# Optimization experiments

Measured on AMD Instinct MI355X. Metric: run time of the kernel, lower is better.

## Reference

```python
import jax, jax.numpy as jnp
import numpy as np

N = 50000      # atoms
E = 800000     # edges (avg degree 32)
H = 64         # hidden_channels
F = 64         # num_filters
G = 50         # num_gaussians
L = 6          # num_interactions
B = 128        # graphs in batch
MAX_Z = 100
CUTOFF = 10.0


def setup_inputs() -> dict:
    key = jax.random.key(0)
    ks = jax.random.split(key, 20)
    s = 0.05  # weight scale
    return {
        "z": jax.random.randint(ks[0], (N,), 0, MAX_Z, dtype=jnp.int32),
        "pos": jax.random.uniform(ks[1], (N, 3), dtype=jnp.float32) * 5.0,
        "batch": jnp.sort(jax.random.randint(ks[2], (N,), 0, B, dtype=jnp.int32)),
        "edge_index": jax.random.randint(ks[3], (2, E), 0, N, dtype=jnp.int32),
        "embed": jax.random.normal(ks[4], (MAX_Z, H), dtype=jnp.float32) * s,
        "mlp_w1": jax.random.normal(ks[5], (L, G, F), dtype=jnp.float32) * s,
        "mlp_b1": jax.random.normal(ks[6], (L, F), dtype=jnp.float32) * s,
        "mlp_w2": jax.random.normal(ks[7], (L, F, F), dtype=jnp.float32) * s,
        "mlp_b2": jax.random.normal(ks[8], (L, F), dtype=jnp.float32) * s,
        "lin_w": jax.random.normal(ks[9], (L, H, F), dtype=jnp.float32) * s,
        "lin_out_w": jax.random.normal(ks[10], (L, F, H), dtype=jnp.float32) * s,
        "lin_out_b": jax.random.normal(ks[11], (L, H), dtype=jnp.float32) * s,
        "fc1_w": jax.random.normal(ks[12], (H, H // 2), dtype=jnp.float32) * s,
        "fc1_b": jax.random.normal(ks[13], (H // 2,), dtype=jnp.float32) * s,
        "fc2_w": jax.random.normal(ks[14], (H // 2, 1), dtype=jnp.float32) * s,
        "fc2_b": jax.random.normal(ks[15], (1,), dtype=jnp.float32) * s,
    }


def reference(z, pos, batch, edge_index, embed, mlp_w1, mlp_b1, mlp_w2, mlp_b2,
              lin_w, lin_out_w, lin_out_b, fc1_w, fc1_b, fc2_w, fc2_b):
    src, dst = edge_index[0], edge_index[1]
    # edge distances (replaces the python cdist loop; edge list is precomputed)
    d = jnp.sqrt(jnp.sum((pos[src] - pos[dst]) ** 2, axis=-1))  # [E]
    # Gaussian smearing
    offset = jnp.linspace(0.0, CUTOFF, G)
    coeff = -0.5 / (offset[1] - offset[0]) ** 2
    edge_attr = jnp.exp(coeff * (d[:, None] - offset) ** 2)  # [E, G]
    # cosine cutoff
    cut = 0.5 * (jnp.cos(d * np.pi / CUTOFF) + 1.0) * (d < CUTOFF).astype(d.dtype)  # [E]

    h = embed[z]  # [N, H]
    for l in range(L):
        # filter MLP on edge features, modulated by cutoff
        W = jnp.tanh(edge_attr @ mlp_w1[l] + mlp_b1[l]) @ mlp_w2[l] + mlp_b2[l]  # [E, F]
        W = W * cut[:, None]
        h_j = h @ lin_w[l]  # [N, F]
        messages = h_j[src] * W  # gather + modulate  [E, F]
        agg = jax.ops.segment_sum(messages, dst, num_segments=N)  # scatter-add [N, F]
        h = h + (agg @ lin_out_w[l] + lin_out_b[l])  # residual

    # global mean pool over graphs
    sums = jax.ops.segment_sum(h, batch, num_segments=B)  # [B, H]
    cnt = jax.ops.segment_sum(jnp.ones((h.shape[0],), h.dtype), batch, num_segments=B)
    pooled = sums / jnp.maximum(cnt, 1.0)[:, None]

    x = jax.nn.relu(pooled @ fc1_w + fc1_b)  # dropout = identity (eval)
    return x @ fc2_w + fc2_b  # [B, 1]
```

## Files before the change

### kernel.cpp

```cpp
#include <hip/hip_runtime.h>
#include <math.h>

#define E_EDGES 800000
#define N_ATOMS 50000
#define N_GRAPH 128
#define P_TBL   4096
#define SCAN_NB 49

static constexpr float PI_F   = 3.14159265358979323846f;
static constexpr float GSTEP  = 10.0f / 49.0f;
static constexpr float GCOEFF = -0.5f / (GSTEP * GSTEP);
static constexpr float DMAX   = 8.6603f;
static constexpr float DSCALE = (float)(P_TBL - 1) / DMAX;

__global__ void hist_kernel(const int* __restrict__ dst, int* __restrict__ cnt) {
    int e = blockIdx.x * 256 + threadIdx.x;
    if (e < E_EDGES) atomicAdd(&cnt[dst[e]], 1);
}

__global__ __launch_bounds__(1024)
void scan1_kernel(const int* __restrict__ cnt, int* __restrict__ local_ex,
                  int* __restrict__ bsum) {
    __shared__ int sh[1024];
    const int t = threadIdx.x;
    const int i = blockIdx.x * 1024 + t;
    const int v = (i < N_ATOMS) ? cnt[i] : 0;
    sh[t] = v;
    __syncthreads();
    #pragma unroll
    for (int off = 1; off < 1024; off <<= 1) {
        int u = (t >= off) ? sh[t - off] : 0;
        __syncthreads();
        sh[t] += u;
        __syncthreads();
    }
    if (i < N_ATOMS) local_ex[i] = sh[t] - v;
    if (t == 1023) bsum[blockIdx.x] = sh[t];
}

__global__ __launch_bounds__(1024)
void scan2_kernel(const int* __restrict__ local_ex, const int* __restrict__ bsum,
                  int* __restrict__ starts, int* __restrict__ cursor) {
    __shared__ int off;
    const int b = blockIdx.x;
    if (threadIdx.x < 64) {
        int v = (threadIdx.x < b) ? bsum[threadIdx.x] : 0;
        #pragma unroll
        for (int d = 32; d > 0; d >>= 1) v += __shfl_down(v, d, 64);
        if (threadIdx.x == 0) off = v;
    }
    __syncthreads();
    const int i = b * 1024 + threadIdx.x;
    if (i < N_ATOMS) {
        int v = local_ex[i] + off;
        starts[i] = v;
        cursor[i] = v;
    }
}

__global__ void scatter_kernel(const int* __restrict__ ei, const float* __restrict__ pos,
                               int* __restrict__ cursor, uint2* __restrict__ pk) {
    int e = blockIdx.x * 256 + threadIdx.x;
    if (e >= E_EDGES) return;
    int sidx = ei[e];
    int dd   = ei[E_EDGES + e];
    float dx = pos[3*sidx+0] - pos[3*dd+0];
    float dy = pos[3*sidx+1] - pos[3*dd+1];
    float dz = pos[3*sidx+2] - pos[3*dd+2];
    float dist = sqrtf(dx*dx + dy*dy + dz*dz);
    int p = atomicAdd(&cursor[dd], 1);
    pk[p] = make_uint2((unsigned)sidx, __float_as_uint(dist));
}

__global__ __launch_bounds__(256)
void table_kernel(const float* __restrict__ w1, const float* __restrict__ b1,
                  const float* __restrict__ w2, const float* __restrict__ b2,
                  float* __restrict__ tbl2) {
    __shared__ float sa[4][52];
    __shared__ float st[4][64];
    const int l  = blockIdx.x >> 10;
    const int rb = blockIdx.x & 1023;
    const int rr = threadIdx.x >> 6;
    const int f  = threadIdx.x & 63;
    const int r  = rb * 4 + rr;
    const float dp = (float)r * (DMAX / (float)(P_TBL - 1));

    if (f < 50) {
        float t = dp - (float)f * GSTEP;
        sa[rr][f] = expf(GCOEFF * t * t);
    }
    __syncthreads();

    const float* W1 = w1 + (size_t)l * 50 * 64;
    const float* W2 = w2 + (size_t)l * 64 * 64;
    float t = b1[l * 64 + f];
    #pragma unroll 5
    for (int g = 0; g < 50; ++g) t = fmaf(sa[rr][g], W1[g * 64 + f], t);
    st[rr][f] = tanhf(t);
    __syncthreads();

    float w = b2[l * 64 + f];
    #pragma unroll 8
    for (int k = 0; k < 64; ++k) w = fmaf(st[rr][k], W2[k * 64 + f], w);
    float cutv = 0.5f * (cosf(dp * (PI_F / 10.0f)) + 1.0f);
    float val = w * cutv;
    const size_t base = ((size_t)l * P_TBL + r) * 64 + f;
    tbl2[base * 2 + 0] = val;
    if (r > 0) tbl2[(base - 64) * 2 + 1] = val;
}

__global__ __launch_bounds__(256)
void embed_lin0_kernel(const int* __restrict__ z, const float* __restrict__ embed,
                       const float* __restrict__ W,
                       float* __restrict__ h, float* __restrict__ hj) {
    __shared__ float sA[64 * 65];
    __shared__ float sW[64 * 64];
    const int tid = threadIdx.x;
    const int rbase = blockIdx.x * 64;

    for (int i = tid; i < 64 * 64; i += 256) sW[i] = W[i];
    for (int i = tid; i < 64 * 64; i += 256) {
        int r = i >> 6, k = i & 63;
        int row = rbase + r;
        float v = 0.0f;
        if (row < N_ATOMS) {
            v = embed[(size_t)z[row] * 64 + k];
            h[(size_t)row * 64 + k] = v;
        }
        sA[r * 65 + k] = v;
    }
    __syncthreads();

    const int f0 = (tid & 7) * 8;
    const int r0 = (tid >> 3) * 2;
    float acc[2][8];
    #pragma unroll
    for (int i = 0; i < 2; ++i)
        #pragma unroll
        for (int j = 0; j < 8; ++j) acc[i][j] = 0.0f;

    #pragma unroll 4
    for (int k = 0; k < 64; ++k) {
        float a[2] = { sA[(r0+0)*65 + k], sA[(r0+1)*65 + k] };
        float4 wa = *(const float4*)&sW[k * 64 + f0];
        float4 wb = *(const float4*)&sW[k * 64 + f0 + 4];
        float w[8] = {wa.x, wa.y, wa.z, wa.w, wb.x, wb.y, wb.z, wb.w};
        #pragma unroll
        for (int i = 0; i < 2; ++i)
            #pragma unroll
            for (int j = 0; j < 8; ++j)
                acc[i][j] = fmaf(a[i], w[j], acc[i][j]);
    }

    #pragma unroll
    for (int i = 0; i < 2; ++i) {
        int row = rbase + r0 + i;
        if (row < N_ATOMS) {
            float* o = hj + (size_t)row * 64;
            *(float4*)&o[f0]     = make_float4(acc[i][0], acc[i][1], acc[i][2], acc[i][3]);
            *(float4*)&o[f0 + 4] = make_float4(acc[i][4], acc[i][5], acc[i][6], acc[i][7]);
        }
    }
}

__device__ __forceinline__ float edge_w2(const float2* __restrict__ tbl, float dist, int f) {
    float x = dist * DSCALE;
    int i0 = (int)x; i0 = (i0 > P_TBL - 2) ? (P_TBL - 2) : i0;
    float fr = x - (float)i0;
    float2 t = tbl[i0 * 64 + f];
    return fmaf(fr, t.y - t.x, t.x);
}

__global__ __launch_bounds__(512)
void layer_kernel(const uint2* __restrict__ pk,
                  const int* __restrict__ starts, const int* __restrict__ cnts,
                  const float* __restrict__ hj_in, const float2* __restrict__ tbl,
                  const float* __restrict__ Wout, const float* __restrict__ bout,
                  float* __restrict__ h,
                  const float* __restrict__ Wlin, float* __restrict__ hj_out,
                  int doLin) {
    __shared__ float sA[64 * 65];
    __shared__ float sW1[64 * 64];
    __shared__ float sW2[64 * 64];
    __shared__ float sb[64];
    const int tid = threadIdx.x;
    const int rbase = blockIdx.x * 64;
    const int f  = tid & 63;
    const int wv = tid >> 6;
    const int r0 = tid >> 3;
    const int f0 = (tid & 7) * 8;
    const int myrow = rbase + r0;

    float4 hA = make_float4(0.f,0.f,0.f,0.f), hB = hA;
    if (myrow < N_ATOMS) {
        const float* hr = h + (size_t)myrow * 64;
        hA = *(const float4*)&hr[f0];
        hB = *(const float4*)&hr[f0 + 4];
    }

    for (int i = tid; i < 64 * 64; i += 512) sW1[i] = Wout[i];
    if (doLin)
        for (int i = tid; i < 64 * 64; i += 512) sW2[i] = Wlin[i];
    if (tid < 64) sb[tid] = bout[tid];
    __syncthreads();

    for (int i = 0; i < 8; ++i) {
        const int r = wv * 8 + i;
        const int n = rbase + r;
        float res = 0.0f;
        if (n < N_ATOMS) {
            const int s   = starts[n];
            const int end = s + cnts[n];
            float a0 = 0.0f, a1 = 0.0f, a2 = 0.0f, a3 = 0.0f;
            float a4 = 0.0f, a5 = 0.0f, a6 = 0.0f, a7 = 0.0f;
            int e = s;
            for (; e + 8 <= end; e += 8) {
                uint2 p0 = pk[e+0], p1 = pk[e+1], p2 = pk[e+2], p3 = pk[e+3];
                uint2 p4 = pk[e+4], p5 = pk[e+5], p6 = pk[e+6], p7 = pk[e+7];
                float w0 = edge_w2(tbl, __uint_as_float(p0.y), f);
                float w1 = edge_w2(tbl, __uint_as_float(p1.y), f);
                float w2 = edge_w2(tbl, __uint_as_float(p2.y), f);
                float w3 = edge_w2(tbl, __uint_as_float(p3.y), f);
                float w4 = edge_w2(tbl, __uint_as_float(p4.y), f);
                float w5 = edge_w2(tbl, __uint_as_float(p5.y), f);
                float w6 = edge_w2(tbl, __uint_as_float(p6.y), f);
                float w7 = edge_w2(tbl, __uint_as_float(p7.y), f);
                a0 = fmaf(w0, hj_in[(size_t)p0.x * 64 + f], a0);
                a1 = fmaf(w1, hj_in[(size_t)p1.x * 64 + f], a1);
                a2 = fmaf(w2, hj_in[(size_t)p2.x * 64 + f], a2);
                a3 = fmaf(w3, hj_in[(size_t)p3.x * 64 + f], a3);
                a4 = fmaf(w4, hj_in[(size_t)p4.x * 64 + f], a4);
                a5 = fmaf(w5, hj_in[(size_t)p5.x * 64 + f], a5);
                a6 = fmaf(w6, hj_in[(size_t)p6.x * 64 + f], a6);
                a7 = fmaf(w7, hj_in[(size_t)p7.x * 64 + f], a7);
            }
            for (; e + 2 <= end; e += 2) {
                uint2 p0 = pk[e], p1 = pk[e+1];
                float w0 = edge_w2(tbl, __uint_as_float(p0.y), f);
                float w1 = edge_w2(tbl, __uint_as_float(p1.y), f);
                a0 = fmaf(w0, hj_in[(size_t)p0.x * 64 + f], a0);
                a1 = fmaf(w1, hj_in[(size_t)p1.x * 64 + f], a1);
            }
            if (e < end) {
                uint2 p0 = pk[e];
                float w0 = edge_w2(tbl, __uint_as_float(p0.y), f);
                a0 = fmaf(w0, hj_in[(size_t)p0.x * 64 + f], a0);
            }
            res = ((a0 + a1) + (a2 + a3)) + ((a4 + a5) + (a6 + a7));
        }
        sA[r * 65 + f] = res;
    }
    __builtin_amdgcn_wave_barrier();

    float acc[8];
    acc[0] = hA.x + sb[f0+0]; acc[1] = hA.y + sb[f0+1];
    acc[2] = hA.z + sb[f0+2]; acc[3] = hA.w + sb[f0+3];
    acc[4] = hB.x + sb[f0+4]; acc[5] = hB.y + sb[f0+5];
    acc[6] = hB.z + sb[f0+6]; acc[7] = hB.w + sb[f0+7];

    #pragma unroll 4
    for (int k = 0; k < 64; ++k) {
        float a = sA[r0 * 65 + k];
        float4 wa = *(const float4*)&sW1[k * 64 + f0];
        float4 wb = *(const float4*)&sW1[k * 64 + f0 + 4];
        acc[0] = fmaf(a, wa.x, acc[0]); acc[1] = fmaf(a, wa.y, acc[1]);
        acc[2] = fmaf(a, wa.z, acc[2]); acc[3] = fmaf(a, wa.w, acc[3]);
        acc[4] = fmaf(a, wb.x, acc[4]); acc[5] = fmaf(a, wb.y, acc[5]);
        acc[6] = fmaf(a, wb.z, acc[6]); acc[7] = fmaf(a, wb.w, acc[7]);
    }
    __builtin_amdgcn_wave_barrier();

    if (myrow < N_ATOMS) {
        float* o = h + (size_t)myrow * 64;
        *(float4*)&o[f0]     = make_float4(acc[0], acc[1], acc[2], acc[3]);
        *(float4*)&o[f0 + 4] = make_float4(acc[4], acc[5], acc[6], acc[7]);
    }
    #pragma unroll
    for (int j = 0; j < 8; ++j) sA[r0 * 65 + f0 + j] = acc[j];
    if (!doLin) return;
    __builtin_amdgcn_wave_barrier();

    float acc2[8];
    #pragma unroll
    for (int j = 0; j < 8; ++j) acc2[j] = 0.0f;

    #pragma unroll 4
    for (int k = 0; k < 64; ++k) {
        float a = sA[r0 * 65 + k];
        float4 wa = *(const float4*)&sW2[k * 64 + f0];
        float4 wb = *(const float4*)&sW2[k * 64 + f0 + 4];
        acc2[0] = fmaf(a, wa.x, acc2[0]); acc2[1] = fmaf(a, wa.y, acc2[1]);
        acc2[2] = fmaf(a, wa.z, acc2[2]); acc2[3] = fmaf(a, wa.w, acc2[3]);
        acc2[4] = fmaf(a, wb.x, acc2[4]); acc2[5] = fmaf(a, wb.y, acc2[5]);
        acc2[6] = fmaf(a, wb.z, acc2[6]); acc2[7] = fmaf(a, wb.w, acc2[7]);
    }

    if (myrow < N_ATOMS) {
        float* o = hj_out + (size_t)myrow * 64;
        *(float4*)&o[f0]     = make_float4(acc2[0], acc2[1], acc2[2], acc2[3]);
        *(float4*)&o[f0 + 4] = make_float4(acc2[4], acc2[5], acc2[6], acc2[7]);
    }
}

__global__ __launch_bounds__(256)
void pool_head_kernel(const float* __restrict__ h, const int* __restrict__ batch,
                      const float* __restrict__ fc1w, const float* __restrict__ fc1b,
                      const float* __restrict__ fc2w, const float* __restrict__ fc2b,
                      float* __restrict__ out) {
    __shared__ float part[4][64];
    __shared__ float sp[64];
    __shared__ float sx[32];
    __shared__ int bounds[2];
    const int g   = blockIdx.x;
    const int tid = threadIdx.x;

    if (tid < 2) {
        int target = g + tid;
        int lo = 0, hi = N_ATOMS;
        while (lo < hi) {
            int m = (lo + hi) >> 1;
            if (batch[m] < target) lo = m + 1; else hi = m;
        }
        bounds[tid] = lo;
    }
    __syncthreads();
    const int s = bounds[0], epos = bounds[1];

    const int f = tid & 63, wv = tid >> 6;
    float a = 0.0f;
    for (int r = s + wv; r < epos; r += 4) a += h[(size_t)r * 64 + f];
    part[wv][f] = a;
    __syncthreads();

    if (tid < 64) {
        float cnt = (float)(epos - s);
        sp[tid] = (part[0][tid] + part[1][tid] + part[2][tid] + part[3][tid])
                  / fmaxf(cnt, 1.0f);
    }
    __syncthreads();
    if (tid < 32) {
        float a1 = fc1b[tid];
        #pragma unroll 8
        for (int k = 0; k < 64; ++k) a1 = fmaf(sp[k], fc1w[k * 32 + tid], a1);
        sx[tid] = fmaxf(a1, 0.0f);
    }
    __syncthreads();
    if (tid == 0) {
        float a2 = fc2b[0];
        #pragma unroll 8
        for (int j = 0; j < 32; ++j) a2 = fmaf(sx[j], fc2w[j], a2);
        out[g] = a2;
    }
}

extern "C" void kernel_launch(void* const* d_in, const int* in_sizes, int n_in,
                              void* d_out, int out_size, void* d_ws, size_t ws_size,
                              hipStream_t stream) {
    const int*   z         = (const int*)  d_in[0];
    const float* pos       = (const float*)d_in[1];
    const int*   batch     = (const int*)  d_in[2];
    const int*   ei        = (const int*)  d_in[3];
    const float* embed     = (const float*)d_in[4];
    const float* mlp_w1    = (const float*)d_in[5];
    const float* mlp_b1    = (const float*)d_in[6];
    const float* mlp_w2    = (const float*)d_in[7];
    const float* mlp_b2    = (const float*)d_in[8];
    const float* lin_w     = (const float*)d_in[9];
    const float* lin_out_w = (const float*)d_in[10];
    const float* lin_out_b = (const float*)d_in[11];
    const float* fc1w      = (const float*)d_in[12];
    const float* fc1b      = (const float*)d_in[13];
    const float* fc2w      = (const float*)d_in[14];
    const float* fc2b      = (const float*)d_in[15];
    float* out = (float*)d_out;

    float*  ws    = (float*)d_ws;
    float*  h     = ws;
    float*  hj0   = h     + (size_t)N_ATOMS * 64;
    float*  hj1   = hj0   + (size_t)N_ATOMS * 64;
    float2* tbl   = (float2*)(hj1 + (size_t)N_ATOMS * 64);
    uint2*  pk    = (uint2*)(tbl + (size_t)6 * P_TBL * 64);
    int*    hist  = (int*)(pk + E_EDGES);
    int*    starts= hist  + N_ATOMS;
    int*    cursor= starts+ N_ATOMS;
    int*    lex   = cursor+ N_ATOMS;
    int*    bsum  = lex   + N_ATOMS;

    const int* dst = ei + E_EDGES;

    hipMemsetAsync(hist, 0, N_ATOMS * sizeof(int), stream);
    hist_kernel<<<E_EDGES / 256, 256, 0, stream>>>(dst, hist);
    scan1_kernel<<<SCAN_NB, 1024, 0, stream>>>(hist, lex, bsum);
    scan2_kernel<<<SCAN_NB, 1024, 0, stream>>>(lex, bsum, starts, cursor);
    scatter_kernel<<<E_EDGES / 256, 256, 0, stream>>>(ei, pos, cursor, pk);
    table_kernel<<<6 * (P_TBL / 4), 256, 0, stream>>>(mlp_w1, mlp_b1, mlp_w2, mlp_b2,
                                                      (float*)tbl);

    const int ngemm_grid = (N_ATOMS + 63) / 64;

    embed_lin0_kernel<<<ngemm_grid, 256, 0, stream>>>(z, embed, lin_w, h, hj0);

    float* hjbuf[2] = { hj0, hj1 };
    for (int l = 0; l < 6; ++l) {
        layer_kernel<<<ngemm_grid, 512, 0, stream>>>(
            pk, starts, hist, hjbuf[l & 1], tbl + (size_t)l * P_TBL * 64,
            lin_out_w + (size_t)l * 64 * 64, lin_out_b + (size_t)l * 64, h,
            (l < 5) ? (lin_w + (size_t)(l + 1) * 64 * 64) : nullptr,
            hjbuf[(l + 1) & 1], (l < 5) ? 1 : 0);
    }

    pool_head_kernel<<<N_GRAPH, 256, 0, stream>>>(h, batch, fc1w, fc1b, fc2w, fc2b, out);
}
```

Before: 729.4 us.

## Store hj features in fp16 and halve the filter lookup table

The per-atom message features hj are now written as fp16 by the embed and layer kernels and widened to fp32 inside the edge gather loop. This halves the bytes moved by the random per-edge gather, which is the dominant memory traffic. The interpolated filter table also drops from 4096 to 2048 distance points, halving table build work and its cache footprint. Both changes cost accuracy: fp16 rounding of the features and coarser linear interpolation of the filter.

```diff
diff --git a/kernel.cpp b/kernel.cpp
--- a/kernel.cpp
+++ b/kernel.cpp
@@ -1,10 +1,11 @@
 #include <hip/hip_runtime.h>
+#include <hip/hip_fp16.h>
 #include <math.h>
 
 #define E_EDGES 800000
 #define N_ATOMS 50000
 #define N_GRAPH 128
-#define P_TBL   4096
+#define P_TBL   2048
 #define SCAN_NB 49
 
 static constexpr float PI_F   = 3.14159265358979323846f;
@@ -78,8 +79,8 @@
                   float* __restrict__ tbl2) {
     __shared__ float sa[4][52];
     __shared__ float st[4][64];
-    const int l  = blockIdx.x >> 10;
-    const int rb = blockIdx.x & 1023;
+    const int l  = blockIdx.x >> 9;
+    const int rb = blockIdx.x & 511;
     const int rr = threadIdx.x >> 6;
     const int f  = threadIdx.x & 63;
     const int r  = rb * 4 + rr;
@@ -109,10 +110,17 @@
     if (r > 0) tbl2[(base - 64) * 2 + 1] = val;
 }
 
+__device__ __forceinline__ void store_half8(__half* dst, const float* v) {
+    union { ushort u[8]; uint4 q; } p;
+    #pragma unroll
+    for (int j = 0; j < 8; ++j) p.u[j] = __half_as_ushort(__float2half(v[j]));
+    *(uint4*)dst = p.q;
+}
+
 __global__ __launch_bounds__(256)
 void embed_lin0_kernel(const int* __restrict__ z, const float* __restrict__ embed,
                        const float* __restrict__ W,
-                       float* __restrict__ h, float* __restrict__ hj) {
+                       float* __restrict__ h, __half* __restrict__ hj) {
     __shared__ float sA[64 * 65];
     __shared__ float sW[64 * 64];
     const int tid = threadIdx.x;
@@ -155,11 +163,8 @@
     #pragma unroll
     for (int i = 0; i < 2; ++i) {
         int row = rbase + r0 + i;
-        if (row < N_ATOMS) {
-            float* o = hj + (size_t)row * 64;
-            *(float4*)&o[f0]     = make_float4(acc[i][0], acc[i][1], acc[i][2], acc[i][3]);
-            *(float4*)&o[f0 + 4] = make_float4(acc[i][4], acc[i][5], acc[i][6], acc[i][7]);
-        }
+        if (row < N_ATOMS)
+            store_half8(hj + (size_t)row * 64 + f0, acc[i]);
     }
 }
 
@@ -174,10 +179,10 @@
 __global__ __launch_bounds__(512)
 void layer_kernel(const uint2* __restrict__ pk,
                   const int* __restrict__ starts, const int* __restrict__ cnts,
-                  const float* __restrict__ hj_in, const float2* __restrict__ tbl,
+                  const __half* __restrict__ hj_in, const float2* __restrict__ tbl,
                   const float* __restrict__ Wout, const float* __restrict__ bout,
                   float* __restrict__ h,
-                  const float* __restrict__ Wlin, float* __restrict__ hj_out,
+                  const float* __restrict__ Wlin, __half* __restrict__ hj_out,
                   int doLin) {
     __shared__ float sA[64 * 65];
     __shared__ float sW1[64 * 64];
@@ -225,26 +230,26 @@
                 float w5 = edge_w2(tbl, __uint_as_float(p5.y), f);
                 float w6 = edge_w2(tbl, __uint_as_float(p6.y), f);
                 float w7 = edge_w2(tbl, __uint_as_float(p7.y), f);
-                a0 = fmaf(w0, hj_in[(size_t)p0.x * 64 + f], a0);
-                a1 = fmaf(w1, hj_in[(size_t)p1.x * 64 + f], a1);
-                a2 = fmaf(w2, hj_in[(size_t)p2.x * 64 + f], a2);
-                a3 = fmaf(w3, hj_in[(size_t)p3.x * 64 + f], a3);
-                a4 = fmaf(w4, hj_in[(size_t)p4.x * 64 + f], a4);
-                a5 = fmaf(w5, hj_in[(size_t)p5.x * 64 + f], a5);
-                a6 = fmaf(w6, hj_in[(size_t)p6.x * 64 + f], a6);
-                a7 = fmaf(w7, hj_in[(size_t)p7.x * 64 + f], a7);
+                a0 = fmaf(w0, __half2float(hj_in[(size_t)p0.x * 64 + f]), a0);
+                a1 = fmaf(w1, __half2float(hj_in[(size_t)p1.x * 64 + f]), a1);
+                a2 = fmaf(w2, __half2float(hj_in[(size_t)p2.x * 64 + f]), a2);
+                a3 = fmaf(w3, __half2float(hj_in[(size_t)p3.x * 64 + f]), a3);
+                a4 = fmaf(w4, __half2float(hj_in[(size_t)p4.x * 64 + f]), a4);
+                a5 = fmaf(w5, __half2float(hj_in[(size_t)p5.x * 64 + f]), a5);
+                a6 = fmaf(w6, __half2float(hj_in[(size_t)p6.x * 64 + f]), a6);
+                a7 = fmaf(w7, __half2float(hj_in[(size_t)p7.x * 64 + f]), a7);
             }
             for (; e + 2 <= end; e += 2) {
                 uint2 p0 = pk[e], p1 = pk[e+1];
                 float w0 = edge_w2(tbl, __uint_as_float(p0.y), f);
                 float w1 = edge_w2(tbl, __uint_as_float(p1.y), f);
-                a0 = fmaf(w0, hj_in[(size_t)p0.x * 64 + f], a0);
-                a1 = fmaf(w1, hj_in[(size_t)p1.x * 64 + f], a1);
+                a0 = fmaf(w0, __half2float(hj_in[(size_t)p0.x * 64 + f]), a0);
+                a1 = fmaf(w1, __half2float(hj_in[(size_t)p1.x * 64 + f]), a1);
             }
             if (e < end) {
                 uint2 p0 = pk[e];
                 float w0 = edge_w2(tbl, __uint_as_float(p0.y), f);
-                a0 = fmaf(w0, hj_in[(size_t)p0.x * 64 + f], a0);
+                a0 = fmaf(w0, __half2float(hj_in[(size_t)p0.x * 64 + f]), a0);
             }
             res = ((a0 + a1) + (a2 + a3)) + ((a4 + a5) + (a6 + a7));
         }
@@ -295,11 +300,8 @@
         acc2[6] = fmaf(a, wb.z, acc2[6]); acc2[7] = fmaf(a, wb.w, acc2[7]);
     }
 
-    if (myrow < N_ATOMS) {
-        float* o = hj_out + (size_t)myrow * 64;
-        *(float4*)&o[f0]     = make_float4(acc2[0], acc2[1], acc2[2], acc2[3]);
-        *(float4*)&o[f0 + 4] = make_float4(acc2[4], acc2[5], acc2[6], acc2[7]);
-    }
+    if (myrow < N_ATOMS)
+        store_half8(hj_out + (size_t)myrow * 64 + f0, acc2);
 }
 
 __global__ __launch_bounds__(256)
@@ -374,11 +376,13 @@
     const float* fc2b      = (const float*)d_in[15];
     float* out = (float*)d_out;
 
-    float*  ws    = (float*)d_ws;
-    float*  h     = ws;
-    float*  hj0   = h     + (size_t)N_ATOMS * 64;
-    float*  hj1   = hj0   + (size_t)N_ATOMS * 64;
-    float2* tbl   = (float2*)(hj1 + (size_t)N_ATOMS * 64);
+    char* base = (char*)d_ws;
+    const size_t HB = (size_t)N_ATOMS * 64 * sizeof(float);
+    const size_t HJ = (size_t)N_ATOMS * 64 * sizeof(__half);
+    float*  h     = (float*)base;
+    __half* hj0   = (__half*)(base + HB);
+    __half* hj1   = (__half*)(base + HB + HJ);
+    float2* tbl   = (float2*)(base + HB + 2 * HJ);
     uint2*  pk    = (uint2*)(tbl + (size_t)6 * P_TBL * 64);
     int*    hist  = (int*)(pk + E_EDGES);
     int*    starts= hist  + N_ATOMS;
@@ -400,7 +404,7 @@
 
     embed_lin0_kernel<<<ngemm_grid, 256, 0, stream>>>(z, embed, lin_w, h, hj0);
 
-    float* hjbuf[2] = { hj0, hj1 };
+    __half* hjbuf[2] = { hj0, hj1 };
     for (int l = 0; l < 6; ++l) {
         layer_kernel<<<ngemm_grid, 512, 0, stream>>>(
             pk, starts, hist, hjbuf[l & 1], tbl + (size_t)l * P_TBL * 64,
```

Result: faster. 707.7 us (-3.0%).
